# Performance work log

Measured on AMD Instinct MI355X. Metric: run time of the kernel, lower is better.

Reference implementation:

```python
import jax, jax.numpy as jnp
import numpy as np

KH, KW = 5, 5


def _patches(x, kh, kw):
    # x: [N, C, H, W] -> [N, C, Ho, Wo, kh*kw] (valid windows)
    N, C, H, W = x.shape
    Ho, Wo = H - kh + 1, W - kw + 1
    return jnp.stack(
        [x[:, :, i:i + Ho, j:j + Wo] for i in range(kh) for j in range(kw)],
        axis=-1,
    )


def setup_inputs() -> dict:
    key = jax.random.key(0)
    k1, k2, k3 = jax.random.split(key, 3)
    inp = jax.random.normal(k1, (4, 2, 256, 256), dtype=jnp.float32)
    filt = jax.random.uniform(k2, (4, 2, KH, KW), dtype=jnp.float32)  # non-negative, like folded-normal init
    p = 0.1 * jax.random.normal(k3, (4, 2), dtype=jnp.float32)
    return {"input": inp, "filter": filt, "p": p}


def reference(input, filter, p):
    # Rescale input to [1, 2] with detached (stop-gradient) min/max
    imin = jax.lax.stop_gradient(jnp.min(input))
    imax = jax.lax.stop_gradient(jnp.max(input))
    x = 1.0 + (input - imin) / (imax - imin)

    O, C, kh, kw = filter.shape
    pats = _patches(x, kh, kw)                      # [N, C, Ho, Wo, K2]
    f = filter.reshape(1, O, C, 1, 1, kh * kw)      # broadcast over N, Ho, Wo
    pe = p.reshape(1, O, C, 1, 1, 1)

    t = pats[:, None] + f                           # [N, O, C, Ho, Wo, K2], t >= 1
    w = t ** pe                                     # t^p
    num = jnp.sum(w * t, axis=(2, 5))               # sum_{c, window} t^(p+1) -> [N, O, Ho, Wo]
    den = jnp.sum(w, axis=(2, 5))                   # sum_{c, window} t^p
    return num / den
```

## Files before the change

### kernel.cpp

```cpp
#include <hip/hip_runtime.h>
#include <float.h>

#define NN 4
#define CC 2
#define HH 256
#define WW 256
#define OO 4
#define KHH 5
#define KWW 5
#define HO 252
#define WO 252

#define TW 32
#define TH 8
#define IW (TW + KWW - 1)
#define IH (TH + KHH - 1)
#define NPART 256
#define BLK 128

typedef float v2f __attribute__((ext_vector_type(2)));

__global__ __launch_bounds__(256) void k_minmax_partial(const float* __restrict__ in,
                                                        float* __restrict__ ws) {
    float vmin = FLT_MAX, vmax = -FLT_MAX;
    const float4* in4 = (const float4*)in;
    #pragma unroll
    for (int k = 0; k < 2; ++k) {
        float4 v = in4[blockIdx.x * 512 + k * 256 + threadIdx.x];
        vmin = fminf(vmin, fminf(fminf(v.x, v.y), fminf(v.z, v.w)));
        vmax = fmaxf(vmax, fmaxf(fmaxf(v.x, v.y), fmaxf(v.z, v.w)));
    }
    #pragma unroll
    for (int off = 32; off > 0; off >>= 1) {
        vmin = fminf(vmin, __shfl_down(vmin, off));
        vmax = fmaxf(vmax, __shfl_down(vmax, off));
    }
    __shared__ float smin[4], smax[4];
    const int wave = threadIdx.x >> 6, lane = threadIdx.x & 63;
    if (lane == 0) { smin[wave] = vmin; smax[wave] = vmax; }
    __syncthreads();
    if (threadIdx.x == 0) {
        ws[2 * blockIdx.x]     = fminf(fminf(smin[0], smin[1]), fminf(smin[2], smin[3]));
        ws[2 * blockIdx.x + 1] = fmaxf(fmaxf(smax[0], smax[1]), fmaxf(smax[2], smax[3]));
    }
}

__global__ __launch_bounds__(BLK) void k_lmorph(const float* __restrict__ in,
                                                const float* __restrict__ filt,
                                                const float* __restrict__ p,
                                                const float* __restrict__ ws,
                                                float* __restrict__ out) {
    const int lane = threadIdx.x & 63;
    const float4* ws4 = (const float4*)ws;
    float4 a = ws4[lane];
    float4 b = ws4[64 + lane];
    float vmin = fminf(fminf(a.x, a.z), fminf(b.x, b.z));
    float vmax = fmaxf(fmaxf(a.y, a.w), fmaxf(b.y, b.w));
    #pragma unroll
    for (int off = 1; off < 64; off <<= 1) {
        vmin = fminf(vmin, __shfl_xor(vmin, off));
        vmax = fmaxf(vmax, __shfl_xor(vmax, off));
    }
    const float gmin = vmin;
    const float inv  = 1.0f / (vmax - vmin);

    __shared__ float xs[CC * IH * IW];
    const int tid = threadIdx.x;
    const int n = blockIdx.z;
    const int y0 = blockIdx.y * TH, x0 = blockIdx.x * TW;

    for (int i = tid; i < CC * IH * IW; i += BLK) {
        int c   = i / (IH * IW);
        int rem = i - c * (IH * IW);
        int r   = rem / IW;
        int col = rem - r * IW;
        int gy = y0 + r, gx = x0 + col;
        float v = 0.0f;
        if (gy < HH && gx < WW) v = in[((n * CC + c) * HH + gy) * WW + gx];
        xs[i] = 1.0f + (v - gmin) * inv;
    }
    __syncthreads();

    const int tx = tid & 15, ty = tid >> 4;
    const int ox0 = x0 + 2 * tx;
    const int oy  = y0 + ty;

    float cf[OO][CC][4];
    #pragma unroll
    for (int o = 0; o < OO; ++o)
        #pragma unroll
        for (int c = 0; c < CC; ++c) {
            const float pp = p[o * CC + c];
            const float s  = exp2f(pp);
            const float b1 = pp;
            const float b2 = 0.5f * pp * (pp - 1.0f);
            const float b3 = b2 * (pp - 2.0f) * (1.0f / 3.0f);
            cf[o][c][3] = s * (0.125f * b3);
            cf[o][c][2] = s * (0.25f * b2 - 0.75f * b3);
            cf[o][c][1] = s * (0.5f * b1 - b2 + 1.5f * b3);
            cf[o][c][0] = s * (1.0f - b1 + b2 - b3);
        }

    v2f numA[OO], numB[OO], denA[OO], denB[OO];
    #pragma unroll
    for (int o = 0; o < OO; ++o) {
        numA[o] = (v2f)(0.0f); numB[o] = (v2f)(0.0f);
        denA[o] = (v2f)(0.0f); denB[o] = (v2f)(0.0f);
    }

    #pragma unroll
    for (int c = 0; c < CC; ++c) {
        float xv[KHH][KWW + 1];
        #pragma unroll
        for (int kh = 0; kh < KHH; ++kh)
            #pragma unroll
            for (int kw = 0; kw < KWW + 1; ++kw)
                xv[kh][kw] = xs[(c * IH + (ty + kh)) * IW + (2 * tx + kw)];

        #pragma unroll
        for (int o = 0; o < OO; ++o) {
            const v2f c0v = (v2f)(cf[o][c][0]);
            const v2f c1v = (v2f)(cf[o][c][1]);
            const v2f c2v = (v2f)(cf[o][c][2]);
            const v2f c3v = (v2f)(cf[o][c][3]);
            #pragma unroll
            for (int kh = 0; kh < KHH; ++kh) {
                #pragma unroll
                for (int kw = 0; kw < KWW; ++kw) {
                    const float f = filt[((o * CC + c) * KHH + kh) * KWW + kw];
                    v2f t;
                    t.x = xv[kh][kw];
                    t.y = xv[kh][kw + 1];
                    t = t + (v2f){f, f};
                    v2f h = t * c3v + c2v;
                    h = t * h + c1v;
                    v2f e = t * h + c0v;
                    if (kh & 1) {
                        numB[o] = e * t + numB[o];
                        denB[o] = denB[o] + e;
                    } else {
                        numA[o] = e * t + numA[o];
                        denA[o] = denA[o] + e;
                    }
                }
            }
        }
    }

    if (oy < HO && ox0 < WO) {
        #pragma unroll
        for (int o = 0; o < OO; ++o) {
            const v2f nu = numA[o] + numB[o];
            const v2f de = denA[o] + denB[o];
            float2 r;
            r.x = nu.x * __builtin_amdgcn_rcpf(de.x);
            r.y = nu.y * __builtin_amdgcn_rcpf(de.y);
            *(float2*)&out[((n * OO + o) * HO + oy) * WO + ox0] = r;
        }
    }
}

extern "C" void kernel_launch(void* const* d_in, const int* in_sizes, int n_in,
                              void* d_out, int out_size, void* d_ws, size_t ws_size,
                              hipStream_t stream) {
    const float* in   = (const float*)d_in[0];
    const float* filt = (const float*)d_in[1];
    const float* p    = (const float*)d_in[2];
    float* out = (float*)d_out;
    float* ws  = (float*)d_ws;

    k_minmax_partial<<<NPART, 256, 0, stream>>>(in, ws);

    dim3 grid((WO + TW - 1) / TW, (HO + TH - 1) / TH, NN);
    k_lmorph<<<grid, BLK, 0, stream>>>(in, filt, p, ws, out);
}
```

Before: 69.72 us.

## Split output channels across blocks and overlap tile load with min/max reduction

The grid now covers output-channel halves, so each block computes two of the four output channels. This doubles the block count (8*32*8 = 2048 blocks), giving more parallelism for a small problem. The input tile is loaded into shared memory before the global min/max reduction and normalized in place afterward, which lets the global loads overlap the workspace reduction. In exchange, each input tile is loaded and normalized twice across blocks.

```diff
diff --git a/kernel.cpp b/kernel.cpp
--- a/kernel.cpp
+++ b/kernel.cpp
@@ -17,6 +17,7 @@
 #define IH (TH + KHH - 1)
 #define NPART 256
 #define BLK 128
+#define OSPLIT 2
 
 typedef float v2f __attribute__((ext_vector_type(2)));
 
@@ -50,7 +51,24 @@
                                                 const float* __restrict__ p,
                                                 const float* __restrict__ ws,
                                                 float* __restrict__ out) {
-    const int lane = threadIdx.x & 63;
+    __shared__ float xs[CC * IH * IW];
+    const int tid = threadIdx.x;
+    const int n  = blockIdx.z >> 1;
+    const int ob = (blockIdx.z & 1) * OSPLIT;
+    const int y0 = blockIdx.y * TH, x0 = blockIdx.x * TW;
+
+    for (int i = tid; i < CC * IH * IW; i += BLK) {
+        int c   = i / (IH * IW);
+        int rem = i - c * (IH * IW);
+        int r   = rem / IW;
+        int col = rem - r * IW;
+        int gy = y0 + r, gx = x0 + col;
+        float v = 0.0f;
+        if (gy < HH && gx < WW) v = in[((n * CC + c) * HH + gy) * WW + gx];
+        xs[i] = v;
+    }
+
+    const int lane = tid & 63;
     const float4* ws4 = (const float4*)ws;
     float4 a = ws4[lane];
     float4 b = ws4[64 + lane];
@@ -64,48 +82,35 @@
     const float gmin = vmin;
     const float inv  = 1.0f / (vmax - vmin);
 
-    __shared__ float xs[CC * IH * IW];
-    const int tid = threadIdx.x;
-    const int n = blockIdx.z;
-    const int y0 = blockIdx.y * TH, x0 = blockIdx.x * TW;
-
-    for (int i = tid; i < CC * IH * IW; i += BLK) {
-        int c   = i / (IH * IW);
-        int rem = i - c * (IH * IW);
-        int r   = rem / IW;
-        int col = rem - r * IW;
-        int gy = y0 + r, gx = x0 + col;
-        float v = 0.0f;
-        if (gy < HH && gx < WW) v = in[((n * CC + c) * HH + gy) * WW + gx];
-        xs[i] = 1.0f + (v - gmin) * inv;
-    }
+    for (int i = tid; i < CC * IH * IW; i += BLK)
+        xs[i] = 1.0f + (xs[i] - gmin) * inv;
     __syncthreads();
 
     const int tx = tid & 15, ty = tid >> 4;
     const int ox0 = x0 + 2 * tx;
     const int oy  = y0 + ty;
 
-    float cf[OO][CC][4];
+    float cf[OSPLIT][CC][4];
     #pragma unroll
-    for (int o = 0; o < OO; ++o)
+    for (int oi = 0; oi < OSPLIT; ++oi)
         #pragma unroll
         for (int c = 0; c < CC; ++c) {
-            const float pp = p[o * CC + c];
+            const float pp = p[(ob + oi) * CC + c];
             const float s  = exp2f(pp);
             const float b1 = pp;
             const float b2 = 0.5f * pp * (pp - 1.0f);
             const float b3 = b2 * (pp - 2.0f) * (1.0f / 3.0f);
-            cf[o][c][3] = s * (0.125f * b3);
-            cf[o][c][2] = s * (0.25f * b2 - 0.75f * b3);
-            cf[o][c][1] = s * (0.5f * b1 - b2 + 1.5f * b3);
-            cf[o][c][0] = s * (1.0f - b1 + b2 - b3);
+            cf[oi][c][3] = s * (0.125f * b3);
+            cf[oi][c][2] = s * (0.25f * b2 - 0.75f * b3);
+            cf[oi][c][1] = s * (0.5f * b1 - b2 + 1.5f * b3);
+            cf[oi][c][0] = s * (1.0f - b1 + b2 - b3);
         }
 
-    v2f numA[OO], numB[OO], denA[OO], denB[OO];
+    v2f numA[OSPLIT], numB[OSPLIT], denA[OSPLIT], denB[OSPLIT];
     #pragma unroll
-    for (int o = 0; o < OO; ++o) {
-        numA[o] = (v2f)(0.0f); numB[o] = (v2f)(0.0f);
-        denA[o] = (v2f)(0.0f); denB[o] = (v2f)(0.0f);
+    for (int oi = 0; oi < OSPLIT; ++oi) {
+        numA[oi] = (v2f)(0.0f); numB[oi] = (v2f)(0.0f);
+        denA[oi] = (v2f)(0.0f); denB[oi] = (v2f)(0.0f);
     }
 
     #pragma unroll
@@ -118,16 +123,16 @@
                 xv[kh][kw] = xs[(c * IH + (ty + kh)) * IW + (2 * tx + kw)];
 
         #pragma unroll
-        for (int o = 0; o < OO; ++o) {
-            const v2f c0v = (v2f)(cf[o][c][0]);
-            const v2f c1v = (v2f)(cf[o][c][1]);
-            const v2f c2v = (v2f)(cf[o][c][2]);
-            const v2f c3v = (v2f)(cf[o][c][3]);
+        for (int oi = 0; oi < OSPLIT; ++oi) {
+            const v2f c0v = (v2f)(cf[oi][c][0]);
+            const v2f c1v = (v2f)(cf[oi][c][1]);
+            const v2f c2v = (v2f)(cf[oi][c][2]);
+            const v2f c3v = (v2f)(cf[oi][c][3]);
             #pragma unroll
             for (int kh = 0; kh < KHH; ++kh) {
                 #pragma unroll
                 for (int kw = 0; kw < KWW; ++kw) {
-                    const float f = filt[((o * CC + c) * KHH + kh) * KWW + kw];
+                    const float f = filt[(((ob + oi) * CC + c) * KHH + kh) * KWW + kw];
                     v2f t;
                     t.x = xv[kh][kw];
                     t.y = xv[kh][kw + 1];
@@ -136,11 +141,11 @@
                     h = t * h + c1v;
                     v2f e = t * h + c0v;
                     if (kh & 1) {
-                        numB[o] = e * t + numB[o];
-                        denB[o] = denB[o] + e;
+                        numB[oi] = e * t + numB[oi];
+                        denB[oi] = denB[oi] + e;
                     } else {
-                        numA[o] = e * t + numA[o];
-                        denA[o] = denA[o] + e;
+                        numA[oi] = e * t + numA[oi];
+                        denA[oi] = denA[oi] + e;
                     }
                 }
             }
@@ -149,13 +154,13 @@
 
     if (oy < HO && ox0 < WO) {
         #pragma unroll
-        for (int o = 0; o < OO; ++o) {
-            const v2f nu = numA[o] + numB[o];
-            const v2f de = denA[o] + denB[o];
+        for (int oi = 0; oi < OSPLIT; ++oi) {
+            const v2f nu = numA[oi] + numB[oi];
+            const v2f de = denA[oi] + denB[oi];
             float2 r;
             r.x = nu.x * __builtin_amdgcn_rcpf(de.x);
             r.y = nu.y * __builtin_amdgcn_rcpf(de.y);
-            *(float2*)&out[((n * OO + o) * HO + oy) * WO + ox0] = r;
+            *(float2*)&out[((n * OO + (ob + oi)) * HO + oy) * WO + ox0] = r;
         }
     }
 }
@@ -171,6 +176,6 @@
 
     k_minmax_partial<<<NPART, 256, 0, stream>>>(in, ws);
 
-    dim3 grid((WO + TW - 1) / TW, (HO + TH - 1) / TH, NN);
+    dim3 grid((WO + TW - 1) / TW, (HO + TH - 1) / TH, NN * (OO / OSPLIT));
     k_lmorph<<<grid, BLK, 0, stream>>>(in, filt, p, ws, out);
 }
```

New measurement: 69.90 us. No clear change (+0.2%).
